# Optimization experiments

Measured on AMD Instinct MI355X. Metric: run time of the kernel, lower is better.

The kernel has to match this reference:

```python
import jax, jax.numpy as jnp
import numpy as np

N_NODES = 100000
DIM = 128
N_REL = 8
N_EDGES = 640000
LAMDA = 1  # indexes into [x, z1, z2]


def setup_inputs() -> dict:
    key = jax.random.key(0)
    ks = jax.random.split(key, 6)
    x = jax.random.normal(ks[0], (N_NODES, DIM), dtype=jnp.float32)
    edge_index = jax.random.randint(ks[1], (2, N_EDGES), 0, N_NODES, dtype=jnp.int32)
    edge_type = jax.random.randint(ks[2], (N_EDGES,), 0, N_REL, dtype=jnp.int32)
    edge_weight = jax.random.uniform(ks[3], (N_EDGES,), dtype=jnp.float32)
    # xavier_uniform for [R, in, out] weight stacks (fan_in=DIM, fan_out=DIM)
    limit = float(np.sqrt(6.0 / (DIM + DIM)))
    W1 = jax.random.uniform(ks[4], (N_REL, DIM, DIM), jnp.float32, -limit, limit)
    W2 = jax.random.uniform(ks[5], (N_REL, DIM, DIM), jnp.float32, -limit, limit)
    b1 = jnp.zeros((DIM,), jnp.float32)
    b2 = jnp.zeros((DIM,), jnp.float32)
    return {"x": x, "edge_index": edge_index, "edge_type": edge_type,
            "edge_weight": edge_weight, "W1": W1, "b1": b1, "W2": W2, "b2": b2}


def _ecge_conv(x, W, b, row, col, edge_type, coef, n_nodes):
    # Faithful to: msg_e = norm_e * w_e * (x[row_e] @ W[type_e]); out = scatter_add(msg, col) + b
    # Efficient form: transform every node by every relation once (N,R,D), then gather per edge.
    xW = jnp.einsum('ni,rio->nro', x, W)          # [N, R, D]
    msg = xW[row, edge_type] * coef[:, None]       # [E, D]
    out = jax.ops.segment_sum(msg, col, num_segments=n_nodes)
    return out + b


def reference(x, edge_index, edge_type, edge_weight, W1, b1, W2, b2):
    n_nodes = x.shape[0]
    row, col = edge_index[0], edge_index[1]
    # symmetric degree normalization based on destination (col) degree
    deg = jax.ops.segment_sum(jnp.ones_like(edge_weight), col, num_segments=n_nodes)
    deg_inv_sqrt = jnp.where(deg > 0, deg ** -0.5, 0.0)
    norm = deg_inv_sqrt[row] * deg_inv_sqrt[col]
    coef = norm * edge_weight

    z1 = jax.nn.relu(_ecge_conv(x, W1, b1, row, col, edge_type, coef, n_nodes))
    # F.dropout with training=False (eval mode) is identity
    z2 = _ecge_conv(z1, W2, b2, row, col, edge_type, coef, n_nodes)

    z_star = (x + z1 + z2) / 4.0
    temp = [x, z1, z2]
    z_sharp = temp[LAMDA]
    for i in range(LAMDA + 1, 3):
        z_sharp = z_sharp + temp[i]
    z_sharp = z_sharp / (4.0 - LAMDA)
    return (z_star, z_sharp)
```

## Files before the change

kernel.cpp:

```cpp
#include <hip/hip_runtime.h>
#include <hip/hip_bf16.h>
#include <cstdint>
#include <cstddef>

#define DIM  128
#define NREL 8
#define SCB  4096
#define CPB  20

typedef __attribute__((ext_vector_type(8))) short short8;
typedef __attribute__((ext_vector_type(4))) float f32x4;

static inline int cdiv(int a, int b){ return (a + b - 1) / b; }

__device__ inline uint32_t packrn(float lo, float hi){
    __hip_bfloat162 h = __float22bfloat162_rn(make_float2(lo, hi));
    union { __hip_bfloat162 h; uint32_t u; } v; v.h = h; return v.u;
}
__device__ inline float bf2f(uint32_t lo16){
    union { uint32_t u; float f; } v; v.u = lo16 << 16; return v.f;
}
__device__ inline float asf(int u){
    union { int i; float f; } v; v.i = u; return v.f;
}

__global__ __launch_bounds__(256) void k_prep(const float* __restrict__ x, unsigned short* __restrict__ xb, int n4,
                                              const int* __restrict__ col, const int* __restrict__ et, int E,
                                              int* __restrict__ cnt8, int nb4, int eb,
                                              const float* __restrict__ W1, const float* __restrict__ W2,
                                              unsigned short* __restrict__ wpk){
    int blk = blockIdx.x;
    if (blk < nb4){
        int i = blk * 256 + threadIdx.x;
        if (i >= n4) return;
        f32x4 v = __builtin_nontemporal_load((const f32x4*)x + i);
        uint2 o; o.x = packrn(v.x, v.y); o.y = packrn(v.z, v.w);
        *(uint2*)(xb + (size_t)i * 4) = o;
    } else if (blk < nb4 + eb){
        int e = (blk - nb4) * 256 + threadIdx.x;
        if (e < E) atomicAdd(&cnt8[col[e] * NREL + et[e]], 1);
    } else {
        int b = (blk - nb4 - eb) * 4 + (threadIdx.x >> 6);
        int lane = threadIdx.x & 63;
        int ks = b & 3, nt = (b >> 2) & 7, slot = b >> 5;
        const float* Wsrc = (slot < 8) ? (W1 + (size_t)slot * DIM * DIM)
                                       : (W2 + (size_t)(slot - 8) * DIM * DIM);
        int k0 = ks * 32 + (lane >> 4) * 8;
        int n  = nt * 16 + (lane & 15);
        uint4 ow;
        ow.x = packrn(Wsrc[(size_t)(k0 + 0) * DIM + n], Wsrc[(size_t)(k0 + 1) * DIM + n]);
        ow.y = packrn(Wsrc[(size_t)(k0 + 2) * DIM + n], Wsrc[(size_t)(k0 + 3) * DIM + n]);
        ow.z = packrn(Wsrc[(size_t)(k0 + 4) * DIM + n], Wsrc[(size_t)(k0 + 5) * DIM + n]);
        ow.w = packrn(Wsrc[(size_t)(k0 + 6) * DIM + n], Wsrc[(size_t)(k0 + 7) * DIM + n]);
        *(uint4*)(wpk + ((size_t)b * 64 + lane) * 8) = ow;
    }
}

__global__ __launch_bounds__(256) void k_scan1(const int* __restrict__ cnt, int M, int* __restrict__ bsum){
    int t = threadIdx.x;
    int base = blockIdx.x * SCB + t * 16;
    int s = 0;
    #pragma unroll
    for (int k = 0; k < 16; ++k){
        int i = base + k;
        if (i < M) s += cnt[i];
    }
    #pragma unroll
    for (int o = 1; o < 64; o <<= 1) s += __shfl_xor(s, o);
    __shared__ int wsum[4];
    if ((t & 63) == 0) wsum[t >> 6] = s;
    __syncthreads();
    if (t == 0) bsum[blockIdx.x] = wsum[0] + wsum[1] + wsum[2] + wsum[3];
}

__global__ __launch_bounds__(256) void k_scan3(const int* __restrict__ cnt, int M,
                                               const int* __restrict__ bsum, int NBS,
                                               int* __restrict__ startArr, int* __restrict__ pos,
                                               float* __restrict__ deginv){
    int t = threadIdx.x;
    int base = blockIdx.x * SCB + t * 16;
    int vals[16];
    int s = 0;
    #pragma unroll
    for (int k = 0; k < 16; ++k){
        int i = base + k;
        vals[k] = (i < M) ? cnt[i] : 0;
        s += vals[k];
    }

    {
        int d0 = 0, d1 = 0;
        #pragma unroll
        for (int k = 0; k < 8; ++k){ d0 += vals[k]; d1 += vals[8 + k]; }
        int c0i = base >> 3;
        if (base < M)     deginv[c0i]     = d0 > 0 ? rsqrtf((float)d0) : 0.f;
        if (base + 8 < M) deginv[c0i + 1] = d1 > 0 ? rsqrtf((float)d1) : 0.f;
    }

    int lane = t & 63, w = t >> 6;

    int bp = 0, tp = 0;
    for (int i = lane; i < NBS; i += 64){
        int bv = bsum[i];
        if (i < (int)blockIdx.x) bp += bv;
        tp += bv;
    }
    #pragma unroll
    for (int o = 1; o < 64; o <<= 1){ bp += __shfl_xor(bp, o); tp += __shfl_xor(tp, o); }

    int v = s;
    #pragma unroll
    for (int o = 1; o < 64; o <<= 1){
        int u = __shfl_up(v, o);
        if (lane >= o) v += u;
    }
    __shared__ int wsum[4];
    if (lane == 63) wsum[w] = v;
    __syncthreads();
    int excl = v - s + bp;
    for (int i = 0; i < w; ++i) excl += wsum[i];
    #pragma unroll
    for (int k = 0; k < 16; ++k){
        int i = base + k;
        if (i < M){ startArr[i] = excl; pos[i] = excl; excl += vals[k]; }
    }
    if (blockIdx.x == (unsigned)(gridDim.x - 1) && t == 0) startArr[M] = tp;
}

__global__ __launch_bounds__(256) void k_place(const int* __restrict__ row, const int* __restrict__ col,
                                               const int* __restrict__ et, const float* __restrict__ ew,
                                               const float* __restrict__ deginv,
                                               int E, int* __restrict__ pos8, int2* __restrict__ pkm){
    int e = blockIdx.x * 256 + threadIdx.x;
    if (e >= E) return;
    int r = row[e], c = col[e], t = et[e];
    float cf = deginv[r] * deginv[c] * ew[e];
    int p = atomicAdd(&pos8[(c << 3) + t], 1);
    int cl = c - (c / CPB) * CPB;
    union { float f; int i; } cv; cv.f = cf;
    pkm[p] = make_int2((cl << 20) | (t << 17) | r, cv.i);
}

template<int MODE>
__global__ __launch_bounds__(512, 8) void k_fused(const unsigned short* __restrict__ xbin,
                                                  const unsigned short* __restrict__ wpk,
                                                  const int* __restrict__ cs8,
                                                  const int2* __restrict__ pkm,
                                                  const float* __restrict__ bias,
                                                  unsigned short* __restrict__ zb,
                                                  const unsigned short* __restrict__ xb2,
                                                  const unsigned short* __restrict__ z1b2,
                                                  float* __restrict__ outS,
                                                  float* __restrict__ outH,
                                                  int N, int wslot){
    __shared__ unsigned short s[CPB * 1024];
    int tid = threadIdx.x;
    int wid = tid >> 6, lane = tid & 63;
    int c0 = blockIdx.x * CPB;
    int nt = wid;
    const short8* bbase = (const short8*)wpk + (size_t)wslot * 2048 + lane;

    uint4 z4 = {0u, 0u, 0u, 0u};
    #pragma unroll
    for (int k = 0; k < 5; ++k) ((uint4*)s)[tid + 512 * k] = z4;
    __syncthreads();

#define FLUSH() *(uint32_t*)((char*)s + flushByte) = packrn(a0, a1)
#define PROC(mx, cf, u) do{                                                       \
        int fk_ = (int)(((unsigned)(mx)) >> 17);                                  \
        if (fk_ != fkPrev){                                                       \
            if (fkPrev >= 0) FLUSH();                                             \
            fkPrev = fk_;                                                         \
            flushByte = (fk_ << 8) + ((lane << 2) ^ ((fk_ << 1) & 0x70));         \
            a0 = 0.f; a1 = 0.f;                                                   \
        }                                                                         \
        a0 = fmaf(cf, bf2f((u) & 0xFFFFu), a0);                                   \
        a1 = fmaf(cf, bf2f((u) >> 16),     a1); }while(0)
#define XROW(mx) ((const uint32_t*)xbin)[((size_t)(((mx) & 0x1FFFF) << 6)) + lane]

    {
        int cLo = c0 + ((wid * CPB) >> 3);
        int cHi = c0 + (((wid + 1) * CPB) >> 3);
        if (cLo > N) cLo = N;
        if (cHi > N) cHi = N;
        if (cLo < cHi){
            int e  = __builtin_amdgcn_readfirstlane(cs8[cLo * NREL]);
            int eE = __builtin_amdgcn_readfirstlane(cs8[cHi * NREL]);
            int fkPrev = -1, flushByte = 0;
            float a0 = 0.f, a1 = 0.f;
            const int* __restrict__ mp = (const int*)pkm;
            while (e < eE){
                int n = eE - e; if (n > 16) n = 16;
                int mxs[16]; float cfs[16]; uint32_t u[16];
                int mprev = 0;
                #pragma unroll
                for (int k = 0; k < 16; ++k){
                    int live = k < n;
                    int raw  = mp[2 * (e + k)];
                    float rc = asf(mp[2 * (e + k) + 1]);
                    int mx = (k == 0) ? raw : (live ? raw : mprev);
                    mxs[k] = mx; mprev = mx;
                    cfs[k] = live ? rc : 0.f;
                }
                #pragma unroll
                for (int k = 0; k < 16; ++k) u[k] = XROW(mxs[k]);
                __builtin_amdgcn_sched_barrier(0);
                #pragma unroll
                for (int k = 0; k < 16; ++k) PROC(mxs[k], cfs[k], u[k]);
                e += n;
            }
            if (fkPrev >= 0) FLUSH();
        }
    }
#undef PROC
#undef FLUSH
#undef XROW

    short8 Bp0 = bbase[(nt * 4 + 0) * 64];
    short8 Bp1 = bbase[(nt * 4 + 1) * 64];
    short8 Bp2 = bbase[(nt * 4 + 2) * 64];
    short8 Bp3 = bbase[(nt * 4 + 3) * 64];
    __syncthreads();

    f32x4 acc0 = (f32x4){0,0,0,0}, acc1 = (f32x4){0,0,0,0};

    int al = lane & 15, ak2 = (lane >> 4) * 16;
    int swz = (al & 7) << 4;
    const char* rowA0 = (const char*)s + al * 2048;
    int r1 = (al < 4) ? (16 + al) : al;
    const char* rowA1 = (const char*)s + r1 * 2048;
    __builtin_amdgcn_s_setprio(1);
    {
        short8 Bp[4] = {Bp0, Bp1, Bp2, Bp3};
        #pragma unroll
        for (int ksl = 0; ksl < 4; ++ksl){
            int off = (ksl * 64 + ak2) ^ swz;
            short8 A0 = *(const short8*)(rowA0 + off);
            short8 A1 = *(const short8*)(rowA1 + off);
            acc0 = __builtin_amdgcn_mfma_f32_16x16x32_bf16(A0, Bp[ksl], acc0, 0, 0, 0);
            acc1 = __builtin_amdgcn_mfma_f32_16x16x32_bf16(A1, Bp[ksl], acc1, 0, 0, 0);
        }
    }
    #pragma unroll 4
    for (int ksg = 4; ksg < 32; ++ksg){
        int off = (ksg * 64 + ak2) ^ swz;
        short8 A0 = *(const short8*)(rowA0 + off);
        short8 A1 = *(const short8*)(rowA1 + off);
        int t = ksg >> 2, ksl = ksg & 3;
        short8 B = (bbase + (size_t)t * 2048)[(nt * 4 + ksl) * 64];
        acc0 = __builtin_amdgcn_mfma_f32_16x16x32_bf16(A0, B, acc0, 0, 0, 0);
        acc1 = __builtin_amdgcn_mfma_f32_16x16x32_bf16(A1, B, acc1, 0, 0, 0);
    }
    __builtin_amdgcn_s_setprio(0);
    __syncthreads();

    float* ot = (float*)s;
    int crb = (lane >> 4) * 4, dcl = lane & 15;
    {
        int d = nt * 16 + dcl;
        float bv = bias[d];
        #pragma unroll
        for (int r = 0; r < 4; ++r){
            int row0 = crb + r;
            float v0 = acc0[r] + bv;
            if (MODE == 0) v0 = fmaxf(v0, 0.f);
            ot[row0 * DIM + d] = v0;
            int row1 = 16 + crb + r;
            if (row1 < CPB){
                float v1 = acc1[r] + bv;
                if (MODE == 0) v1 = fmaxf(v1, 0.f);
                ot[row1 * DIM + d] = v1;
            }
        }
    }
    __syncthreads();

    if (MODE == 0){
        if (tid < CPB * 16){
            int rowi = tid >> 4, seg = tid & 15;
            int c = c0 + rowi;
            if (c < N){
                const float* src = ot + rowi * DIM + seg * 8;
                uint4 vv;
                vv.x = packrn(src[0], src[1]);
                vv.y = packrn(src[2], src[3]);
                vv.z = packrn(src[4], src[5]);
                vv.w = packrn(src[6], src[7]);
                *(uint4*)(zb + ((size_t)c << 7) + seg * 8) = vv;
            }
        }
    } else {
        #pragma unroll
        for (int pass = 0; pass < 2; ++pass){
            int rowi = (pass == 0) ? (tid >> 5) : (16 + (tid >> 5));
            bool act = (pass == 0) || (tid < (CPB - 16) * 32);
            int c = c0 + rowi;
            if (act && c < N){
                int q = tid & 31;
                int d0 = q * 4;
                size_t o = ((size_t)c << 7) + d0;
                ushort4 xv4 = *(const ushort4*)(xb2 + o);
                ushort4 zv4 = *(const ushort4*)(z1b2 + o);
                const float* src = ot + rowi * DIM + d0;
                f32x4 S, H;
                {
                    float xv = bf2f(xv4.x), z1 = bf2f(zv4.x), v = src[0];
                    S.x = (xv + z1 + v) * 0.25f; H.x = (z1 + v) * (1.0f / 3.0f);
                }
                {
                    float xv = bf2f(xv4.y), z1 = bf2f(zv4.y), v = src[1];
                    S.y = (xv + z1 + v) * 0.25f; H.y = (z1 + v) * (1.0f / 3.0f);
                }
                {
                    float xv = bf2f(xv4.z), z1 = bf2f(zv4.z), v = src[2];
                    S.z = (xv + z1 + v) * 0.25f; H.z = (z1 + v) * (1.0f / 3.0f);
                }
                {
                    float xv = bf2f(xv4.w), z1 = bf2f(zv4.w), v = src[3];
                    S.w = (xv + z1 + v) * 0.25f; H.w = (z1 + v) * (1.0f / 3.0f);
                }
                __builtin_nontemporal_store(S, (f32x4*)(outS + o));
                __builtin_nontemporal_store(H, (f32x4*)(outH + o));
            }
        }
    }
}

extern "C" void kernel_launch(void* const* d_in, const int* in_sizes, int n_in,
                              void* d_out, int out_size, void* d_ws, size_t ws_size,
                              hipStream_t stream) {
    const float* x  = (const float*)d_in[0];
    const int*   ei = (const int*)d_in[1];
    const int*   et = (const int*)d_in[2];
    const float* ew = (const float*)d_in[3];
    const float* W1 = (const float*)d_in[4];
    const float* b1 = (const float*)d_in[5];
    const float* W2 = (const float*)d_in[6];
    const float* b2 = (const float*)d_in[7];

    int E = in_sizes[2];
    int N = in_sizes[0] / DIM;
    const int* row = ei;
    const int* col = ei + E;

    float* out = (float*)d_out;
    int ND  = N * DIM;
    int ND4 = ND / 4;
    float* zS = out;
    float* zH = out + ND;

    int M8   = N * NREL;
    int NBS8 = cdiv(M8, SCB);

    char* wsb = (char*)d_ws;
    size_t off = 0;
    auto take = [&](size_t bytes) -> char* {
        char* p = wsb + off;
        off = (off + bytes + 255) & ~(size_t)255;
        return p;
    };
    int*            cnt8     = (int*)           take((size_t)M8 * 4);
    int*            start8   = (int*)           take(((size_t)M8 + 1) * 4);
    int*            pos8     = (int*)           take((size_t)M8 * 4);
    int*            bsum     = (int*)           take(((size_t)NBS8 + 1) * 4);
    float*          deginv   = (float*)         take((size_t)N * 4);
    int2*           pkm      = (int2*)          take(((size_t)E + 16) * 8);
    unsigned short* wpk      = (unsigned short*)take((size_t)16 * 2048 * 8 * 2);
    unsigned short* xb       = (unsigned short*)take((size_t)ND * 2);
    unsigned short* z1b      = (unsigned short*)take((size_t)ND * 2);
    (void)n_in; (void)out_size; (void)ws_size;

    (void)hipMemsetAsync(cnt8, 0, (size_t)M8 * 4, stream);

    int eb  = cdiv(E, 256);
    int nb4 = cdiv(ND4, 256);
    k_prep  <<<nb4 + eb + 128, 256, 0, stream>>>(x, xb, ND4, col, et, E, cnt8, nb4, eb, W1, W2, wpk);
    k_scan1 <<<NBS8, 256, 0, stream>>>(cnt8, M8, bsum);
    k_scan3 <<<NBS8, 256, 0, stream>>>(cnt8, M8, bsum, NBS8, start8, pos8, deginv);
    k_place <<<eb, 256, 0, stream>>>(row, col, et, ew, deginv, E, pos8, pkm);

    int fb = cdiv(N, CPB);
    k_fused<0><<<fb, 512, 0, stream>>>(xb, wpk, start8, pkm, b1, z1b, nullptr, nullptr, nullptr, nullptr, N, 0);
    k_fused<1><<<fb, 512, 0, stream>>>(z1b, wpk, start8, pkm, b2, nullptr, xb, z1b, zS, zH, N, 8);
}
```

Baseline: 247.4 us.

## Merge preprocessing kernels into one persistent kernel with grid-wide barriers

Replaces the memset, prep, two scan kernels and placement kernel with a single launch. The first 512 blocks clear counts, histogram, scan and place edges, separated by atomic-counter grid barriers. The remaining blocks convert weights and x to bf16 concurrently. This removes several launch gaps and lets the bf16 conversion overlap the CSR build. It relies on all 512 barrier blocks being co-resident; the extra conversion blocks could delay their scheduling, and the spin barriers add cost of their own.

```diff
diff --git a/kernel.cpp b/kernel.cpp
--- a/kernel.cpp
+++ b/kernel.cpp
@@ -5,8 +5,9 @@
 
 #define DIM  128
 #define NREL 8
-#define SCB  4096
 #define CPB  20
+#define GB   512
+#define CVB  2048
 
 typedef __attribute__((ext_vector_type(8))) short short8;
 typedef __attribute__((ext_vector_type(4))) float f32x4;
@@ -24,121 +25,124 @@
     union { int i; float f; } v; v.i = u; return v.f;
 }
 
-__global__ __launch_bounds__(256) void k_prep(const float* __restrict__ x, unsigned short* __restrict__ xb, int n4,
-                                              const int* __restrict__ col, const int* __restrict__ et, int E,
-                                              int* __restrict__ cnt8, int nb4, int eb,
+__device__ inline void gsync(int* c, int target){
+    __syncthreads();
+    __threadfence();
+    if (threadIdx.x == 0){
+        atomicAdd(c, 1);
+        while (atomicAdd(c, 0) < target) __builtin_amdgcn_s_sleep(8);
+    }
+    __syncthreads();
+    __threadfence();
+}
+
+__global__ __launch_bounds__(256) void k_mega(const float* __restrict__ x, unsigned short* __restrict__ xb, int n4,
+                                              const int* __restrict__ row, const int* __restrict__ col,
+                                              const int* __restrict__ et, const float* __restrict__ ew,
                                               const float* __restrict__ W1, const float* __restrict__ W2,
-                                              unsigned short* __restrict__ wpk){
+                                              unsigned short* __restrict__ wpk,
+                                              int* __restrict__ cnt8, int M8,
+                                              int* __restrict__ bsum, int* __restrict__ startArr,
+                                              int* __restrict__ pos8, float* __restrict__ deginv,
+                                              int2* __restrict__ pkm, int E,
+                                              int* __restrict__ sync){
     int blk = blockIdx.x;
-    if (blk < nb4){
-        int i = blk * 256 + threadIdx.x;
-        if (i >= n4) return;
-        f32x4 v = __builtin_nontemporal_load((const f32x4*)x + i);
-        uint2 o; o.x = packrn(v.x, v.y); o.y = packrn(v.z, v.w);
-        *(uint2*)(xb + (size_t)i * 4) = o;
-    } else if (blk < nb4 + eb){
-        int e = (blk - nb4) * 256 + threadIdx.x;
-        if (e < E) atomicAdd(&cnt8[col[e] * NREL + et[e]], 1);
-    } else {
-        int b = (blk - nb4 - eb) * 4 + (threadIdx.x >> 6);
-        int lane = threadIdx.x & 63;
-        int ks = b & 3, nt = (b >> 2) & 7, slot = b >> 5;
-        const float* Wsrc = (slot < 8) ? (W1 + (size_t)slot * DIM * DIM)
-                                       : (W2 + (size_t)(slot - 8) * DIM * DIM);
-        int k0 = ks * 32 + (lane >> 4) * 8;
-        int n  = nt * 16 + (lane & 15);
-        uint4 ow;
-        ow.x = packrn(Wsrc[(size_t)(k0 + 0) * DIM + n], Wsrc[(size_t)(k0 + 1) * DIM + n]);
-        ow.y = packrn(Wsrc[(size_t)(k0 + 2) * DIM + n], Wsrc[(size_t)(k0 + 3) * DIM + n]);
-        ow.z = packrn(Wsrc[(size_t)(k0 + 4) * DIM + n], Wsrc[(size_t)(k0 + 5) * DIM + n]);
-        ow.w = packrn(Wsrc[(size_t)(k0 + 6) * DIM + n], Wsrc[(size_t)(k0 + 7) * DIM + n]);
-        *(uint4*)(wpk + ((size_t)b * 64 + lane) * 8) = ow;
-    }
-}
-
-__global__ __launch_bounds__(256) void k_scan1(const int* __restrict__ cnt, int M, int* __restrict__ bsum){
-    int t = threadIdx.x;
-    int base = blockIdx.x * SCB + t * 16;
-    int s = 0;
+    int tid = threadIdx.x;
+
+    if (blk >= GB){
+        if (blk < GB + 128){
+            int b = (blk - GB) * 4 + (tid >> 6);
+            int lane = tid & 63;
+            int ks = b & 3, nt = (b >> 2) & 7, slot = b >> 5;
+            const float* Wsrc = (slot < 8) ? (W1 + (size_t)slot * DIM * DIM)
+                                           : (W2 + (size_t)(slot - 8) * DIM * DIM);
+            int k0 = ks * 32 + (lane >> 4) * 8;
+            int n  = nt * 16 + (lane & 15);
+            uint4 ow;
+            ow.x = packrn(Wsrc[(size_t)(k0 + 0) * DIM + n], Wsrc[(size_t)(k0 + 1) * DIM + n]);
+            ow.y = packrn(Wsrc[(size_t)(k0 + 2) * DIM + n], Wsrc[(size_t)(k0 + 3) * DIM + n]);
+            ow.z = packrn(Wsrc[(size_t)(k0 + 4) * DIM + n], Wsrc[(size_t)(k0 + 5) * DIM + n]);
+            ow.w = packrn(Wsrc[(size_t)(k0 + 6) * DIM + n], Wsrc[(size_t)(k0 + 7) * DIM + n]);
+            *(uint4*)(wpk + ((size_t)b * 64 + lane) * 8) = ow;
+        } else {
+            int cb = blk - GB - 128;
+            for (int i = cb * 256 + tid; i < n4; i += CVB * 256){
+                f32x4 v = __builtin_nontemporal_load((const f32x4*)x + i);
+                uint2 o; o.x = packrn(v.x, v.y); o.y = packrn(v.z, v.w);
+                *(uint2*)(xb + (size_t)i * 4) = o;
+            }
+        }
+        return;
+    }
+
+    __shared__ int wsum[4];
+    int lane = tid & 63, w = tid >> 6;
+
+    for (int i = blk * 256 + tid; i < M8; i += GB * 256) cnt8[i] = 0;
+    gsync(sync + 0, GB);
+
+    for (int e = blk * 256 + tid; e < E; e += GB * 256)
+        atomicAdd(&cnt8[(col[e] << 3) + et[e]], 1);
+    gsync(sync + 1, GB);
+
+    int base = (blk * 256 + tid) * 8;
+    int vals[8]; int s = 0;
     #pragma unroll
-    for (int k = 0; k < 16; ++k){
+    for (int k = 0; k < 8; ++k){
         int i = base + k;
-        if (i < M) s += cnt[i];
-    }
-    #pragma unroll
-    for (int o = 1; o < 64; o <<= 1) s += __shfl_xor(s, o);
-    __shared__ int wsum[4];
-    if ((t & 63) == 0) wsum[t >> 6] = s;
-    __syncthreads();
-    if (t == 0) bsum[blockIdx.x] = wsum[0] + wsum[1] + wsum[2] + wsum[3];
-}
-
-__global__ __launch_bounds__(256) void k_scan3(const int* __restrict__ cnt, int M,
-                                               const int* __restrict__ bsum, int NBS,
-                                               int* __restrict__ startArr, int* __restrict__ pos,
-                                               float* __restrict__ deginv){
-    int t = threadIdx.x;
-    int base = blockIdx.x * SCB + t * 16;
-    int vals[16];
-    int s = 0;
-    #pragma unroll
-    for (int k = 0; k < 16; ++k){
-        int i = base + k;
-        vals[k] = (i < M) ? cnt[i] : 0;
+        vals[k] = (i < M8) ? cnt8[i] : 0;
         s += vals[k];
     }
-
-    {
-        int d0 = 0, d1 = 0;
-        #pragma unroll
-        for (int k = 0; k < 8; ++k){ d0 += vals[k]; d1 += vals[8 + k]; }
-        int c0i = base >> 3;
-        if (base < M)     deginv[c0i]     = d0 > 0 ? rsqrtf((float)d0) : 0.f;
-        if (base + 8 < M) deginv[c0i + 1] = d1 > 0 ? rsqrtf((float)d1) : 0.f;
-    }
-
-    int lane = t & 63, w = t >> 6;
-
-    int bp = 0, tp = 0;
-    for (int i = lane; i < NBS; i += 64){
-        int bv = bsum[i];
-        if (i < (int)blockIdx.x) bp += bv;
-        tp += bv;
-    }
-    #pragma unroll
-    for (int o = 1; o < 64; o <<= 1){ bp += __shfl_xor(bp, o); tp += __shfl_xor(tp, o); }
-
-    int v = s;
-    #pragma unroll
-    for (int o = 1; o < 64; o <<= 1){
-        int u = __shfl_up(v, o);
-        if (lane >= o) v += u;
-    }
-    __shared__ int wsum[4];
-    if (lane == 63) wsum[w] = v;
-    __syncthreads();
-    int excl = v - s + bp;
-    for (int i = 0; i < w; ++i) excl += wsum[i];
-    #pragma unroll
-    for (int k = 0; k < 16; ++k){
-        int i = base + k;
-        if (i < M){ startArr[i] = excl; pos[i] = excl; excl += vals[k]; }
-    }
-    if (blockIdx.x == (unsigned)(gridDim.x - 1) && t == 0) startArr[M] = tp;
-}
-
-__global__ __launch_bounds__(256) void k_place(const int* __restrict__ row, const int* __restrict__ col,
-                                               const int* __restrict__ et, const float* __restrict__ ew,
-                                               const float* __restrict__ deginv,
-                                               int E, int* __restrict__ pos8, int2* __restrict__ pkm){
-    int e = blockIdx.x * 256 + threadIdx.x;
-    if (e >= E) return;
-    int r = row[e], c = col[e], t = et[e];
-    float cf = deginv[r] * deginv[c] * ew[e];
-    int p = atomicAdd(&pos8[(c << 3) + t], 1);
-    int cl = c - (c / CPB) * CPB;
-    union { float f; int i; } cv; cv.f = cf;
-    pkm[p] = make_int2((cl << 20) | (t << 17) | r, cv.i);
+    if (base < M8) deginv[base >> 3] = s > 0 ? rsqrtf((float)s) : 0.f;
+    {
+        int ws = s;
+        #pragma unroll
+        for (int o = 1; o < 64; o <<= 1) ws += __shfl_xor(ws, o);
+        if (lane == 0) wsum[w] = ws;
+        __syncthreads();
+        if (tid == 0) bsum[blk] = wsum[0] + wsum[1] + wsum[2] + wsum[3];
+    }
+    gsync(sync + 2, GB);
+
+    {
+        int NBS = (M8 + 2047) >> 11;
+        int bp = 0, tp = 0;
+        for (int i = lane; i < NBS; i += 64){
+            int bv = bsum[i];
+            if (i < blk) bp += bv;
+            tp += bv;
+        }
+        #pragma unroll
+        for (int o = 1; o < 64; o <<= 1){ bp += __shfl_xor(bp, o); tp += __shfl_xor(tp, o); }
+
+        int v = s;
+        #pragma unroll
+        for (int o = 1; o < 64; o <<= 1){
+            int u = __shfl_up(v, o);
+            if (lane >= o) v += u;
+        }
+        __syncthreads();
+        if (lane == 63) wsum[w] = v;
+        __syncthreads();
+        int excl = v - s + bp;
+        for (int i = 0; i < w; ++i) excl += wsum[i];
+        #pragma unroll
+        for (int k = 0; k < 8; ++k){
+            int i = base + k;
+            if (i < M8){ startArr[i] = excl; pos8[i] = excl; excl += vals[k]; }
+        }
+        if (blk == 0 && tid == 0) startArr[M8] = tp;
+    }
+    gsync(sync + 3, GB);
+
+    for (int e = blk * 256 + tid; e < E; e += GB * 256){
+        int r = row[e], c = col[e], t = et[e];
+        float cf = deginv[r] * deginv[c] * ew[e];
+        int p = atomicAdd(&pos8[(c << 3) + t], 1);
+        int cl = c - (c / CPB) * CPB;
+        union { float f; int i; } cv; cv.f = cf;
+        pkm[p] = make_int2((cl << 20) | (t << 17) | r, cv.i);
+    }
 }
 
 template<int MODE>
@@ -229,6 +233,7 @@
     const char* rowA0 = (const char*)s + al * 2048;
     int r1 = (al < 4) ? (16 + al) : al;
     const char* rowA1 = (const char*)s + r1 * 2048;
+
     __builtin_amdgcn_s_setprio(1);
     {
         short8 Bp[4] = {Bp0, Bp1, Bp2, Bp3};
@@ -349,8 +354,7 @@
     float* zS = out;
     float* zH = out + ND;
 
-    int M8   = N * NREL;
-    int NBS8 = cdiv(M8, SCB);
+    int M8 = N * NREL;
 
     char* wsb = (char*)d_ws;
     size_t off = 0;
@@ -362,22 +366,20 @@
     int*            cnt8     = (int*)           take((size_t)M8 * 4);
     int*            start8   = (int*)           take(((size_t)M8 + 1) * 4);
     int*            pos8     = (int*)           take((size_t)M8 * 4);
-    int*            bsum     = (int*)           take(((size_t)NBS8 + 1) * 4);
+    int*            bsum     = (int*)           take(((size_t)GB + 1) * 4);
     float*          deginv   = (float*)         take((size_t)N * 4);
+    int*            syncCnt  = (int*)           take(64);
     int2*           pkm      = (int2*)          take(((size_t)E + 16) * 8);
     unsigned short* wpk      = (unsigned short*)take((size_t)16 * 2048 * 8 * 2);
     unsigned short* xb       = (unsigned short*)take((size_t)ND * 2);
     unsigned short* z1b      = (unsigned short*)take((size_t)ND * 2);
     (void)n_in; (void)out_size; (void)ws_size;
 
-    (void)hipMemsetAsync(cnt8, 0, (size_t)M8 * 4, stream);
-
-    int eb  = cdiv(E, 256);
-    int nb4 = cdiv(ND4, 256);
-    k_prep  <<<nb4 + eb + 128, 256, 0, stream>>>(x, xb, ND4, col, et, E, cnt8, nb4, eb, W1, W2, wpk);
-    k_scan1 <<<NBS8, 256, 0, stream>>>(cnt8, M8, bsum);
-    k_scan3 <<<NBS8, 256, 0, stream>>>(cnt8, M8, bsum, NBS8, start8, pos8, deginv);
-    k_place <<<eb, 256, 0, stream>>>(row, col, et, ew, deginv, E, pos8, pkm);
+    (void)hipMemsetAsync(syncCnt, 0, 16, stream);
+
+    k_mega<<<GB + 128 + CVB, 256, 0, stream>>>(x, xb, ND4, row, col, et, ew, W1, W2, wpk,
+                                               cnt8, M8, bsum, start8, pos8, deginv, pkm, E,
+                                               syncCnt);
 
     int fb = cdiv(N, CPB);
     k_fused<0><<<fb, 512, 0, stream>>>(xb, wpk, start8, pkm, b1, z1b, nullptr, nullptr, nullptr, nullptr, N, 0);
```

Result: slower. 669.9 us (+170.7%).
